# Performance work log

Hardware: AMD Instinct MI355X
Metric: run time of the kernel (lower is better)

Reference implementation:

```python
import jax, jax.numpy as jnp
import numpy as np

N_NODES = 50000
N_EDGES = 800000
D_IN, D_HID, D_OUT = 96, 96, 32


def setup_inputs() -> dict:
    key = jax.random.key(0)
    ks = jax.random.split(key, 8)
    x = jax.random.normal(ks[0], (N_NODES, D_IN), dtype=jnp.float32)
    edge_index = jax.random.randint(ks[1], (2, N_EDGES), 0, N_NODES, dtype=jnp.int64)
    # Glorot-style init for GCNConv linear weights, zero bias (PyG default)
    def glorot(k, fan_in, fan_out):
        s = jnp.sqrt(6.0 / (fan_in + fan_out))
        return jax.random.uniform(k, (fan_in, fan_out), jnp.float32, -s, s)
    return {
        "x": x,
        "edge_index": edge_index,
        "W1": glorot(ks[2], D_IN, D_HID), "b1": jnp.zeros((D_HID,), jnp.float32),
        "W2": glorot(ks[3], D_HID, D_HID), "b2": jnp.zeros((D_HID,), jnp.float32),
        "W3": glorot(ks[4], D_HID, D_OUT), "b3": jnp.zeros((D_OUT,), jnp.float32),
    }


def _gcn_conv(x, W, b, src, dst, norm, n):
    # x: [N, d_in] -> transform then normalized neighbor aggregation (incl. self-loops)
    h = x @ W                                   # [N, d_out]
    msgs = h[src] * norm[:, None]               # [E+N, d_out] gather + scale
    out = jax.ops.segment_sum(msgs, dst, num_segments=n)  # scatter-add
    return out + b


def reference(x, edge_index, W1, b1, W2, b2, W3, b3):
    n = x.shape[0]
    loop = jnp.arange(n, dtype=edge_index.dtype)
    src = jnp.concatenate([edge_index[0], loop])  # [E+N]
    dst = jnp.concatenate([edge_index[1], loop])  # [E+N]
    # symmetric GCN normalization: deg^-1/2[src] * deg^-1/2[dst] (self-loops included)
    deg = jax.ops.segment_sum(jnp.ones_like(dst, dtype=x.dtype), dst, num_segments=n)
    dinv = jnp.where(deg > 0, jax.lax.rsqrt(deg), 0.0)
    norm = dinv[src] * dinv[dst]

    h = jax.nn.relu(_gcn_conv(x, W1, b1, src, dst, norm, n))  # dropout: eval mode (identity)
    h = jax.nn.relu(_gcn_conv(h, W2, b2, src, dst, norm, n))
    return _gcn_conv(h, W3, b3, src, dst, norm, n)
```

## Files before the change

### kernel.cpp

```cpp
#include <hip/hip_runtime.h>
#include <hip/hip_bf16.h>
#include <hip/hip_fp16.h>

static constexpr int KDIM = 96;
static constexpr int BSH = 7;
static constexpr int BNODES = 1 << BSH;
static constexpr int MAXBK = 400;

typedef _Float16 f16x8 __attribute__((ext_vector_type(8)));
typedef float f32x4 __attribute__((ext_vector_type(4)));

__device__ __forceinline__ void gemm96_f32_body(const float* __restrict__ x,
                                                const float* __restrict__ Wg,
                                                __half* __restrict__ out, int N,
                                                int gb, char* sm) {
  _Float16* Wt = (_Float16*)sm;
  const int tid = threadIdx.x;
  for (int i = tid; i < 96 * 96; i += 256) {
    int k = i / 96, j = i - k * 96;
    Wt[j * 104 + k] = (_Float16)Wg[i];
  }
  __syncthreads();
  const int wave = tid >> 6;
  const int l = tid & 63;
  const int crow = l & 15;
  const int kgrp = l >> 4;
  int r = gb * 64 + wave * 16 + crow;
  int rc = (r < N) ? r : (N - 1);
  f16x8 a[3];
  const float* ap = x + (size_t)rc * 96 + kgrp * 8;
#pragma unroll
  for (int ks = 0; ks < 3; ++ks) {
    float4 u = *(const float4*)(ap + ks * 32);
    float4 w = *(const float4*)(ap + ks * 32 + 4);
    a[ks][0] = (_Float16)u.x; a[ks][1] = (_Float16)u.y;
    a[ks][2] = (_Float16)u.z; a[ks][3] = (_Float16)u.w;
    a[ks][4] = (_Float16)w.x; a[ks][5] = (_Float16)w.y;
    a[ks][6] = (_Float16)w.z; a[ks][7] = (_Float16)w.w;
  }
  const int rbase = gb * 64 + wave * 16 + kgrp * 4;
#pragma unroll
  for (int nt = 0; nt < 6; ++nt) {
    f32x4 c = {0.f, 0.f, 0.f, 0.f};
#pragma unroll
    for (int ks = 0; ks < 3; ++ks) {
      f16x8 b = *(const f16x8*)&Wt[(nt * 16 + crow) * 104 + ks * 32 + kgrp * 8];
      c = __builtin_amdgcn_mfma_f32_16x16x32_f16(a[ks], b, c, 0, 0, 0);
    }
#pragma unroll
    for (int reg = 0; reg < 4; ++reg) {
      int R = rbase + reg;
      if (R < N) out[(size_t)R * 96 + nt * 16 + crow] = (__half)c[reg];
    }
  }
}

__global__ __launch_bounds__(256) void khist_gemm1(const int* __restrict__ dst,
                                                   int* __restrict__ gbcnt,
                                                   int E, int NBK,
                                                   const float* __restrict__ x,
                                                   const float* __restrict__ W1,
                                                   __half* __restrict__ tA, int N,
                                                   const float* __restrict__ W2,
                                                   const float* __restrict__ W3,
                                                   _Float16* __restrict__ Wt2,
                                                   _Float16* __restrict__ Wt3,
                                                   int gG) {
  __shared__ __align__(16) char sm[96 * 104 * 2];
  if (blockIdx.x < 256) {
    int* h = (int*)sm;
    for (int i = threadIdx.x; i < NBK; i += 256) h[i] = 0;
    __syncthreads();
    for (int e = blockIdx.x * 256 + threadIdx.x; e < E; e += 256 * 256)
      atomicAdd(&h[dst[e] >> BSH], 1);
    __syncthreads();
    for (int i = threadIdx.x; i < NBK; i += 256)
      if (h[i]) atomicAdd(&gbcnt[i], h[i]);
  } else if (blockIdx.x < 256 + gG) {
    gemm96_f32_body(x, W1, tA, N, blockIdx.x - 256, sm);
  } else {
    for (int i = threadIdx.x; i < 96 * 96; i += 256) {
      int k = i / 96, j = i - k * 96;
      Wt2[j * 96 + k] = (_Float16)W2[i];
    }
    for (int i = threadIdx.x; i < 96 * 32; i += 256) {
      int k = i / 32, j = i - k * 32;
      Wt3[j * 96 + k] = (_Float16)W3[i];
    }
  }
}

__global__ void kb_scanb(const int* __restrict__ gbcnt, int* __restrict__ bstart,
                         int* __restrict__ bcur, int NBK) {
  __shared__ int s[512];
  int t = threadIdx.x;
  int v = (t < NBK) ? gbcnt[t] : 0;
  s[t] = v;
  __syncthreads();
  for (int o = 1; o < 512; o <<= 1) {
    int a = (t >= o) ? s[t - o] : 0;
    __syncthreads();
    s[t] += a;
    __syncthreads();
  }
  if (t < NBK) {
    int excl = s[t] - v;
    bstart[t] = excl;
    bcur[t] = excl;
  }
  if (t == 511) bstart[NBK] = s[511];
}

__global__ __launch_bounds__(256) void kb_scatter(const int* __restrict__ src,
                                                  const int* __restrict__ dst,
                                                  int* __restrict__ bcur,
                                                  unsigned* __restrict__ tmp,
                                                  int E, int NBK, int chunk) {
  __shared__ int h[MAXBK];
  __shared__ int base[MAXBK];
  int lo = blockIdx.x * chunk;
  int hi = min(lo + chunk, E);
  for (int i = threadIdx.x; i < NBK; i += 256) h[i] = 0;
  __syncthreads();
  for (int e = lo + threadIdx.x; e < hi; e += 256) atomicAdd(&h[dst[e] >> BSH], 1);
  __syncthreads();
  for (int i = threadIdx.x; i < NBK; i += 256) {
    int c = h[i];
    base[i] = c ? atomicAdd(&bcur[i], c) : 0;
    h[i] = 0;
  }
  __syncthreads();
  for (int e = lo + threadIdx.x; e < hi; e += 256) {
    int d = dst[e];
    int b = d >> BSH;
    int p = base[b] + atomicAdd(&h[b], 1);
    tmp[p] = (unsigned)src[e] | ((unsigned)(d & (BNODES - 1)) << 16);
  }
}

__global__ __launch_bounds__(256) void kb_cnt2(const unsigned* __restrict__ tmp,
                                               const int* __restrict__ bstart,
                                               int* __restrict__ cursor,
                                               float* __restrict__ dinv,
                                               int2* __restrict__ rs, int N) {
  __shared__ int hcnt[BNODES];
  __shared__ int scn[BNODES];
  __shared__ int gbs;
  int b = blockIdx.x;
  int t = threadIdx.x;
  for (int i = t; i < BNODES; i += 256) hcnt[i] = 0;
  __syncthreads();
  int lo = bstart[b], hi = bstart[b + 1];
  for (int p = lo + t; p < hi; p += 256)
    atomicAdd(&hcnt[(tmp[p] >> 16) & (BNODES - 1)], 1);
  __syncthreads();
  int pcnt = 0;
  if (t < BNODES) {
    pcnt = (hcnt[t] + 3) & ~3;
    scn[t] = pcnt;
  }
  __syncthreads();
  for (int o = 1; o < BNODES; o <<= 1) {
    int a = (t < BNODES && t >= o) ? scn[t - o] : 0;
    __syncthreads();
    if (t < BNODES) scn[t] += a;
    __syncthreads();
  }
  if (t == 0) gbs = atomicAdd(cursor, scn[BNODES - 1]);
  __syncthreads();
  if (t < BNODES) {
    int v = (b << BSH) + t;
    if (v < N) {
      int beg = gbs + scn[t] - pcnt;
      rs[v] = make_int2(beg, beg + pcnt);
      dinv[v] = rsqrtf((float)hcnt[t] + 1.0f);
    }
  }
}

__global__ __launch_bounds__(256) void kb_final2(const unsigned* __restrict__ tmp,
                                                 const int* __restrict__ bstart,
                                                 const int2* __restrict__ rs,
                                                 const float* __restrict__ dinv,
                                                 unsigned* __restrict__ ew, int N) {
  __shared__ int beg[BNODES];
  __shared__ int endp[BNODES];
  __shared__ int lcur[BNODES];
  int b = blockIdx.x;
  int t = threadIdx.x;
  int v0 = b << BSH;
  if (t < BNODES) {
    int v = v0 + t;
    if (v < N) {
      int2 r = rs[v];
      beg[t] = r.x;
      endp[t] = r.y;
    } else {
      beg[t] = 0;
      endp[t] = 0;
    }
    lcur[t] = 0;
  }
  __syncthreads();
  int lo = bstart[b], hi = bstart[b + 1];
  for (int p = lo + t; p < hi; p += 256) {
    unsigned u = tmp[p];
    int dl = (u >> 16) & (BNODES - 1);
    int s = u & 0xFFFF;
    int pos = beg[dl] + atomicAdd(&lcur[dl], 1);
    unsigned hw = (unsigned)__half_as_ushort(__float2half(dinv[s]));
    ew[pos] = (unsigned)s | (hw << 16);
  }
  __syncthreads();
  if (t < BNODES) {
    int p = beg[t] + lcur[t];
    int end = endp[t];
    for (; p < end; ++p) ew[p] = 0u;
  }
}

template <int DOUT>
__global__ __launch_bounds__(256) void kfuse(const __half* __restrict__ t,
                                             const int2* __restrict__ rs,
                                             const unsigned* __restrict__ ew,
                                             const float* __restrict__ dinv,
                                             const float* __restrict__ bias,
                                             const _Float16* __restrict__ Wt,
                                             __half* __restrict__ out, int N) {
  __shared__ _Float16 A[16 * 104];
  const int tid = threadIdx.x;
  const int wave = tid >> 6;
  const int lane = tid & 63;
  const int li = (lane < 48) ? lane : 47;
  const int fb = li << 2;
  const char* tb = (const char*)t;
  const float bx = bias[2 * li];
  const float by = bias[2 * li + 1];
#pragma unroll
  for (int i = 0; i < 4; ++i) {
    int row = wave * 4 + i;
    int v = blockIdx.x * 16 + row;
    if (v < N) {
      float dv = dinv[v];
      float2 acc;
      {
        __half2 r = *(const __half2*)(tb + (size_t)v * 192 + fb);
        float2 f = __half22float2(r);
        acc.x = dv * f.x;
        acc.y = dv * f.y;
      }
      int2 range = rs[v];
      int e = range.x;
      const int e1 = range.y;
      for (; e < e1; e += 4) {
        uint4 q = *(const uint4*)(ew + e);
        __half2 r0 = *(const __half2*)(tb + (size_t)(q.x & 0xFFFF) * 192 + fb);
        __half2 r1 = *(const __half2*)(tb + (size_t)(q.y & 0xFFFF) * 192 + fb);
        __half2 r2 = *(const __half2*)(tb + (size_t)(q.z & 0xFFFF) * 192 + fb);
        __half2 r3 = *(const __half2*)(tb + (size_t)(q.w & 0xFFFF) * 192 + fb);
        float2 a0 = __half22float2(r0), a1 = __half22float2(r1);
        float2 a2 = __half22float2(r2), a3 = __half22float2(r3);
        float w0 = __half2float(__ushort_as_half((unsigned short)(q.x >> 16)));
        float w1 = __half2float(__ushort_as_half((unsigned short)(q.y >> 16)));
        float w2 = __half2float(__ushort_as_half((unsigned short)(q.z >> 16)));
        float w3 = __half2float(__ushort_as_half((unsigned short)(q.w >> 16)));
        acc.x = fmaf(w0, a0.x, acc.x); acc.y = fmaf(w0, a0.y, acc.y);
        acc.x = fmaf(w1, a1.x, acc.x); acc.y = fmaf(w1, a1.y, acc.y);
        acc.x = fmaf(w2, a2.x, acc.x); acc.y = fmaf(w2, a2.y, acc.y);
        acc.x = fmaf(w3, a3.x, acc.x); acc.y = fmaf(w3, a3.y, acc.y);
      }
      if (lane < 48) {
        float rx = fmaxf(fmaf(dv, acc.x, bx), 0.f);
        float ry = fmaxf(fmaf(dv, acc.y, by), 0.f);
        A[row * 104 + 2 * li] = (_Float16)rx;
        A[row * 104 + 2 * li + 1] = (_Float16)ry;
      }
    }
  }
  __syncthreads();
  const int crow = lane & 15;
  const int kgrp = lane >> 4;
  f16x8 a[3];
  const _Float16* arow = &A[crow * 104 + kgrp * 8];
#pragma unroll
  for (int ks = 0; ks < 3; ++ks) a[ks] = *(const f16x8*)(arow + ks * 32);
  const int rbase = blockIdx.x * 16 + kgrp * 4;
#pragma unroll
  for (int w2 = 0; w2 < 2; ++w2) {
    int nt = wave + 4 * w2;
    if (nt >= DOUT / 16) break;
    f32x4 c = {0.f, 0.f, 0.f, 0.f};
#pragma unroll
    for (int ks = 0; ks < 3; ++ks) {
      f16x8 b = *(const f16x8*)&Wt[(nt * 16 + crow) * 96 + ks * 32 + kgrp * 8];
      c = __builtin_amdgcn_mfma_f32_16x16x32_f16(a[ks], b, c, 0, 0, 0);
    }
#pragma unroll
    for (int reg = 0; reg < 4; ++reg) {
      int R = rbase + reg;
      if (R < N) out[(size_t)R * DOUT + nt * 16 + crow] = (__half)c[reg];
    }
  }
}

__global__ __launch_bounds__(256) void k_agg32h(const __half* __restrict__ t,
                                                const int2* __restrict__ rs,
                                                const unsigned* __restrict__ ew,
                                                const float* __restrict__ dinv,
                                                const float* __restrict__ bias,
                                                float* __restrict__ out, int N) {
  int half = threadIdx.x >> 5;
  int lane = threadIdx.x & 31;
  int v = blockIdx.x * 8 + half;
  if (v >= N) return;
  const char* tb = (const char*)t;
  const int fb = lane << 1;
  float dv = dinv[v];
  float acc = dv * __half2float(*(const __half*)(tb + (size_t)v * 64 + fb));
  int2 range = rs[v];
  int e = range.x;
  const int e1 = range.y;
  for (; e < e1; e += 4) {
    uint4 q = *(const uint4*)(ew + e);
    float a0 = __half2float(*(const __half*)(tb + (size_t)(q.x & 0xFFFF) * 64 + fb));
    float a1 = __half2float(*(const __half*)(tb + (size_t)(q.y & 0xFFFF) * 64 + fb));
    float a2 = __half2float(*(const __half*)(tb + (size_t)(q.z & 0xFFFF) * 64 + fb));
    float a3 = __half2float(*(const __half*)(tb + (size_t)(q.w & 0xFFFF) * 64 + fb));
    acc = fmaf(__half2float(__ushort_as_half((unsigned short)(q.x >> 16))), a0, acc);
    acc = fmaf(__half2float(__ushort_as_half((unsigned short)(q.y >> 16))), a1, acc);
    acc = fmaf(__half2float(__ushort_as_half((unsigned short)(q.z >> 16))), a2, acc);
    acc = fmaf(__half2float(__ushort_as_half((unsigned short)(q.w >> 16))), a3, acc);
  }
  out[(size_t)v * 32 + lane] = fmaf(dv, acc, bias[lane]);
}


extern "C" void kernel_launch(void* const* d_in, const int* in_sizes, int n_in,
                              void* d_out, int out_size, void* d_ws, size_t ws_size,
                              hipStream_t stream) {
  const float* x  = (const float*)d_in[0];
  const int*   ei = (const int*)d_in[1];
  const float* W1 = (const float*)d_in[2];
  const float* b1 = (const float*)d_in[3];
  const float* W2 = (const float*)d_in[4];
  const float* b2 = (const float*)d_in[5];
  const float* W3 = (const float*)d_in[6];
  const float* b3 = (const float*)d_in[7];
  float* out = (float*)d_out;

  const int N = in_sizes[0] / KDIM;
  const int E = in_sizes[1] / 2;
  const int* src = ei;
  const int* dst = ei + E;
  const int NBK = (N + BNODES - 1) >> BSH;

  char* w = (char*)d_ws;
  size_t off = 0;
  auto alloc = [&](size_t bytes) {
    char* p = w + off;
    off = (off + bytes + 255) & ~(size_t)255;
    return p;
  };
  int*       gbcnt    = (int*)alloc((size_t)(MAXBK + 8) * 4);
  int*       bstart   = (int*)alloc((size_t)(MAXBK + 1) * 4);
  int*       bcur     = (int*)alloc((size_t)MAXBK * 4);
  float*     dinv     = (float*)alloc((size_t)N * 4);
  int2*      rs       = (int2*)alloc((size_t)N * 8);
  unsigned*  tmp      = (unsigned*)alloc((size_t)E * 4);
  unsigned*  ew       = (unsigned*)alloc((size_t)(E + 4 * (size_t)N + 16) * 4);
  __half*    tA       = (__half*)alloc((size_t)N * KDIM * 2);
  __half*    tB       = (__half*)alloc((size_t)N * KDIM * 2);
  __half*    tC       = (__half*)alloc((size_t)N * 32 * 2);
  _Float16*  Wt2      = (_Float16*)alloc((size_t)96 * 96 * 2);
  _Float16*  Wt3      = (_Float16*)alloc((size_t)32 * 96 * 2);
  int*       cursor   = gbcnt + MAXBK;

  hipMemsetAsync(gbcnt, 0, (size_t)(MAXBK + 8) * 4, stream);

  const int NCH = 512;
  const int chunk = (E + NCH - 1) / NCH;
  const int gG = (N + 63) / 64;
  const int gF = (N + 15) / 16;
  const int gA8 = (N + 7) / 8;

  khist_gemm1<<<256 + gG + 1, 256, 0, stream>>>(dst, gbcnt, E, NBK, x, W1, tA, N,
                                                W2, W3, Wt2, Wt3, gG);
  kb_scanb<<<1, 512, 0, stream>>>(gbcnt, bstart, bcur, NBK);
  kb_scatter<<<NCH, 256, 0, stream>>>(src, dst, bcur, tmp, E, NBK, chunk);
  kb_cnt2<<<NBK, 256, 0, stream>>>(tmp, bstart, cursor, dinv, rs, N);
  kb_final2<<<NBK, 256, 0, stream>>>(tmp, bstart, rs, dinv, ew, N);

  kfuse<96><<<gF, 256, 0, stream>>>(tA, rs, ew, dinv, b1, Wt2, tB, N);
  kfuse<32><<<gF, 256, 0, stream>>>(tB, rs, ew, dinv, b2, Wt3, tC, N);
  k_agg32h<<<gA8, 256, 0, stream>>>(tC, rs, ew, dinv, b3, out, N);
}
```

Baseline: 161.5 us.

## Replace bucket histogram+scan with fixed-capacity buckets and global per-node counts

Removes the separate bucket histogram, scan, and count kernels by scattering edges directly into fixed-capacity per-bucket regions (CAP slots each). Per-node degrees come from global atomics during the scatter, which is fused with the first GEMM launch. A per-256-node scan kernel then builds row starts. This cuts three launches and one pass over the edge list, at the cost of heavy global atomic traffic on node counters. It also risks overflow if a bucket ever exceeds CAP edges.

```diff
diff --git a/kernel.cpp b/kernel.cpp
--- a/kernel.cpp
+++ b/kernel.cpp
@@ -6,6 +6,7 @@
 static constexpr int BSH = 7;
 static constexpr int BNODES = 1 << BSH;
 static constexpr int MAXBK = 400;
+static constexpr int CAP = 4096;
 
 typedef _Float16 f16x8 __attribute__((ext_vector_type(8)));
 typedef float f32x4 __attribute__((ext_vector_type(4)));
@@ -55,29 +56,43 @@
   }
 }
 
-__global__ __launch_bounds__(256) void khist_gemm1(const int* __restrict__ dst,
-                                                   int* __restrict__ gbcnt,
-                                                   int E, int NBK,
-                                                   const float* __restrict__ x,
-                                                   const float* __restrict__ W1,
-                                                   __half* __restrict__ tA, int N,
-                                                   const float* __restrict__ W2,
-                                                   const float* __restrict__ W3,
-                                                   _Float16* __restrict__ Wt2,
-                                                   _Float16* __restrict__ Wt3,
-                                                   int gG) {
+__global__ __launch_bounds__(256) void ksca_gemm1(
+    const int* __restrict__ src, const int* __restrict__ dst,
+    int* __restrict__ cnt, int* __restrict__ bcur, unsigned* __restrict__ tmp,
+    int E, int NBK, int chunk,
+    const float* __restrict__ x, const float* __restrict__ W1,
+    __half* __restrict__ tA, int N,
+    const float* __restrict__ W2, const float* __restrict__ W3,
+    _Float16* __restrict__ Wt2, _Float16* __restrict__ Wt3,
+    int NCH, int gG) {
   __shared__ __align__(16) char sm[96 * 104 * 2];
-  if (blockIdx.x < 256) {
+  if (blockIdx.x < (unsigned)NCH) {
     int* h = (int*)sm;
+    int* base = h + MAXBK;
+    int lo = blockIdx.x * chunk;
+    int hi = min(lo + chunk, E);
     for (int i = threadIdx.x; i < NBK; i += 256) h[i] = 0;
     __syncthreads();
-    for (int e = blockIdx.x * 256 + threadIdx.x; e < E; e += 256 * 256)
-      atomicAdd(&h[dst[e] >> BSH], 1);
-    __syncthreads();
-    for (int i = threadIdx.x; i < NBK; i += 256)
-      if (h[i]) atomicAdd(&gbcnt[i], h[i]);
-  } else if (blockIdx.x < 256 + gG) {
-    gemm96_f32_body(x, W1, tA, N, blockIdx.x - 256, sm);
+    for (int e = lo + threadIdx.x; e < hi; e += 256) {
+      int d = dst[e];
+      atomicAdd(&h[d >> BSH], 1);
+      atomicAdd(&cnt[d], 1);
+    }
+    __syncthreads();
+    for (int i = threadIdx.x; i < NBK; i += 256) {
+      int c = h[i];
+      base[i] = c ? (i * CAP + atomicAdd(&bcur[i], c)) : 0;
+      h[i] = 0;
+    }
+    __syncthreads();
+    for (int e = lo + threadIdx.x; e < hi; e += 256) {
+      int d = dst[e];
+      int b = d >> BSH;
+      int p = base[b] + atomicAdd(&h[b], 1);
+      tmp[p] = (unsigned)src[e] | ((unsigned)(d & (BNODES - 1)) << 16);
+    }
+  } else if (blockIdx.x < (unsigned)(NCH + gG)) {
+    gemm96_f32_body(x, W1, tA, N, blockIdx.x - NCH, sm);
   } else {
     for (int i = threadIdx.x; i < 96 * 96; i += 256) {
       int k = i / 96, j = i - k * 96;
@@ -90,96 +105,35 @@
   }
 }
 
-__global__ void kb_scanb(const int* __restrict__ gbcnt, int* __restrict__ bstart,
-                         int* __restrict__ bcur, int NBK) {
-  __shared__ int s[512];
+__global__ __launch_bounds__(256) void k_rs(const int* __restrict__ cnt,
+                                            int* __restrict__ cursor,
+                                            float* __restrict__ dinv,
+                                            int2* __restrict__ rs, int N) {
+  __shared__ int scn[256];
+  __shared__ int gbs;
   int t = threadIdx.x;
-  int v = (t < NBK) ? gbcnt[t] : 0;
-  s[t] = v;
-  __syncthreads();
-  for (int o = 1; o < 512; o <<= 1) {
-    int a = (t >= o) ? s[t - o] : 0;
-    __syncthreads();
-    s[t] += a;
-    __syncthreads();
-  }
-  if (t < NBK) {
-    int excl = s[t] - v;
-    bstart[t] = excl;
-    bcur[t] = excl;
-  }
-  if (t == 511) bstart[NBK] = s[511];
-}
-
-__global__ __launch_bounds__(256) void kb_scatter(const int* __restrict__ src,
-                                                  const int* __restrict__ dst,
-                                                  int* __restrict__ bcur,
-                                                  unsigned* __restrict__ tmp,
-                                                  int E, int NBK, int chunk) {
-  __shared__ int h[MAXBK];
-  __shared__ int base[MAXBK];
-  int lo = blockIdx.x * chunk;
-  int hi = min(lo + chunk, E);
-  for (int i = threadIdx.x; i < NBK; i += 256) h[i] = 0;
-  __syncthreads();
-  for (int e = lo + threadIdx.x; e < hi; e += 256) atomicAdd(&h[dst[e] >> BSH], 1);
-  __syncthreads();
-  for (int i = threadIdx.x; i < NBK; i += 256) {
-    int c = h[i];
-    base[i] = c ? atomicAdd(&bcur[i], c) : 0;
-    h[i] = 0;
-  }
-  __syncthreads();
-  for (int e = lo + threadIdx.x; e < hi; e += 256) {
-    int d = dst[e];
-    int b = d >> BSH;
-    int p = base[b] + atomicAdd(&h[b], 1);
-    tmp[p] = (unsigned)src[e] | ((unsigned)(d & (BNODES - 1)) << 16);
-  }
-}
-
-__global__ __launch_bounds__(256) void kb_cnt2(const unsigned* __restrict__ tmp,
-                                               const int* __restrict__ bstart,
-                                               int* __restrict__ cursor,
-                                               float* __restrict__ dinv,
-                                               int2* __restrict__ rs, int N) {
-  __shared__ int hcnt[BNODES];
-  __shared__ int scn[BNODES];
-  __shared__ int gbs;
-  int b = blockIdx.x;
-  int t = threadIdx.x;
-  for (int i = t; i < BNODES; i += 256) hcnt[i] = 0;
-  __syncthreads();
-  int lo = bstart[b], hi = bstart[b + 1];
-  for (int p = lo + t; p < hi; p += 256)
-    atomicAdd(&hcnt[(tmp[p] >> 16) & (BNODES - 1)], 1);
-  __syncthreads();
-  int pcnt = 0;
-  if (t < BNODES) {
-    pcnt = (hcnt[t] + 3) & ~3;
-    scn[t] = pcnt;
-  }
-  __syncthreads();
-  for (int o = 1; o < BNODES; o <<= 1) {
-    int a = (t < BNODES && t >= o) ? scn[t - o] : 0;
-    __syncthreads();
-    if (t < BNODES) scn[t] += a;
-    __syncthreads();
-  }
-  if (t == 0) gbs = atomicAdd(cursor, scn[BNODES - 1]);
-  __syncthreads();
-  if (t < BNODES) {
-    int v = (b << BSH) + t;
-    if (v < N) {
-      int beg = gbs + scn[t] - pcnt;
-      rs[v] = make_int2(beg, beg + pcnt);
-      dinv[v] = rsqrtf((float)hcnt[t] + 1.0f);
-    }
-  }
-}
-
-__global__ __launch_bounds__(256) void kb_final2(const unsigned* __restrict__ tmp,
-                                                 const int* __restrict__ bstart,
+  int v = blockIdx.x * 256 + t;
+  int c = (v < N) ? cnt[v] : 0;
+  int p = (c + 3) & ~3;
+  scn[t] = p;
+  __syncthreads();
+  for (int o = 1; o < 256; o <<= 1) {
+    int a = (t >= o) ? scn[t - o] : 0;
+    __syncthreads();
+    scn[t] += a;
+    __syncthreads();
+  }
+  if (t == 0) gbs = atomicAdd(cursor, scn[255]);
+  __syncthreads();
+  if (v < N) {
+    int beg = gbs + scn[t] - p;
+    rs[v] = make_int2(beg, beg + p);
+    dinv[v] = rsqrtf((float)c + 1.0f);
+  }
+}
+
+__global__ __launch_bounds__(256) void kb_final3(const unsigned* __restrict__ tmp,
+                                                 const int* __restrict__ bcur,
                                                  const int2* __restrict__ rs,
                                                  const float* __restrict__ dinv,
                                                  unsigned* __restrict__ ew, int N) {
@@ -202,9 +156,10 @@
     lcur[t] = 0;
   }
   __syncthreads();
-  int lo = bstart[b], hi = bstart[b + 1];
-  for (int p = lo + t; p < hi; p += 256) {
-    unsigned u = tmp[p];
+  const unsigned* tb = tmp + (size_t)b * CAP;
+  int cntb = bcur[b];
+  for (int p = t; p < cntb; p += 256) {
+    unsigned u = tb[p];
     int dl = (u >> 16) & (BNODES - 1);
     int s = u & 0xFFFF;
     int pos = beg[dl] + atomicAdd(&lcur[dl], 1);
@@ -361,21 +316,21 @@
     off = (off + bytes + 255) & ~(size_t)255;
     return p;
   };
-  int*       gbcnt    = (int*)alloc((size_t)(MAXBK + 8) * 4);
-  int*       bstart   = (int*)alloc((size_t)(MAXBK + 1) * 4);
-  int*       bcur     = (int*)alloc((size_t)MAXBK * 4);
+  int*       meta     = (int*)alloc((size_t)(MAXBK + 8 + N) * 4);
+  int*       bcur     = meta;
+  int*       cursor   = meta + MAXBK;
+  int*       cnt      = meta + MAXBK + 8;
   float*     dinv     = (float*)alloc((size_t)N * 4);
   int2*      rs       = (int2*)alloc((size_t)N * 8);
-  unsigned*  tmp      = (unsigned*)alloc((size_t)E * 4);
+  unsigned*  tmp      = (unsigned*)alloc((size_t)MAXBK * CAP * 4);
   unsigned*  ew       = (unsigned*)alloc((size_t)(E + 4 * (size_t)N + 16) * 4);
   __half*    tA       = (__half*)alloc((size_t)N * KDIM * 2);
   __half*    tB       = (__half*)alloc((size_t)N * KDIM * 2);
   __half*    tC       = (__half*)alloc((size_t)N * 32 * 2);
   _Float16*  Wt2      = (_Float16*)alloc((size_t)96 * 96 * 2);
   _Float16*  Wt3      = (_Float16*)alloc((size_t)32 * 96 * 2);
-  int*       cursor   = gbcnt + MAXBK;
-
-  hipMemsetAsync(gbcnt, 0, (size_t)(MAXBK + 8) * 4, stream);
+
+  hipMemsetAsync(meta, 0, (size_t)(MAXBK + 8 + N) * 4, stream);
 
   const int NCH = 512;
   const int chunk = (E + NCH - 1) / NCH;
@@ -383,12 +338,11 @@
   const int gF = (N + 15) / 16;
   const int gA8 = (N + 7) / 8;
 
-  khist_gemm1<<<256 + gG + 1, 256, 0, stream>>>(dst, gbcnt, E, NBK, x, W1, tA, N,
-                                                W2, W3, Wt2, Wt3, gG);
-  kb_scanb<<<1, 512, 0, stream>>>(gbcnt, bstart, bcur, NBK);
-  kb_scatter<<<NCH, 256, 0, stream>>>(src, dst, bcur, tmp, E, NBK, chunk);
-  kb_cnt2<<<NBK, 256, 0, stream>>>(tmp, bstart, cursor, dinv, rs, N);
-  kb_final2<<<NBK, 256, 0, stream>>>(tmp, bstart, rs, dinv, ew, N);
+  ksca_gemm1<<<NCH + gG + 1, 256, 0, stream>>>(src, dst, cnt, bcur, tmp, E, NBK,
+                                               chunk, x, W1, tA, N, W2, W3, Wt2,
+                                               Wt3, NCH, gG);
+  k_rs<<<(N + 255) / 256, 256, 0, stream>>>(cnt, cursor, dinv, rs, N);
+  kb_final3<<<NBK, 256, 0, stream>>>(tmp, bcur, rs, dinv, ew, N);
 
   kfuse<96><<<gF, 256, 0, stream>>>(tA, rs, ew, dinv, b1, Wt2, tB, N);
   kfuse<32><<<gF, 256, 0, stream>>>(tB, rs, ew, dinv, b2, Wt3, tC, N);
```

Measured after the change: 179.0 us. +10.9%, slower.

## Fuse CSR build kernels and shrink edge list to 16-bit indices

Applied to the files above, without the earlier changes.

Merges the count and fill kernels into one build kernel, which drops a launch and a second pass over the bucketed temp array. The packed 32-bit edge entries (source index plus half-precision source weight) become bare 16-bit source indices. Aggregation kernels now look up the source normalisation in a small half-precision dinv table. Padding slots point at sentinel node N, whose weight is zero, and the feature buffers get an extra row for it. This halves edge-list traffic at the cost of an extra cached gather per edge; the sentinel feature rows are never initialised, so a NaN there could leak through the zero weight.

```diff
diff --git a/kernel.cpp b/kernel.cpp
--- a/kernel.cpp
+++ b/kernel.cpp
@@ -91,7 +91,8 @@
 }
 
 __global__ void kb_scanb(const int* __restrict__ gbcnt, int* __restrict__ bstart,
-                         int* __restrict__ bcur, int NBK) {
+                         int* __restrict__ bcur, int NBK,
+                         __half* __restrict__ dinv16, int N) {
   __shared__ int s[512];
   int t = threadIdx.x;
   int v = (t < NBK) ? gbcnt[t] : 0;
@@ -109,6 +110,7 @@
     bcur[t] = excl;
   }
   if (t == 511) bstart[NBK] = s[511];
+  if (t == 0) dinv16[N] = __ushort_as_half((unsigned short)0);
 }
 
 __global__ __launch_bounds__(256) void kb_scatter(const int* __restrict__ src,
@@ -138,13 +140,18 @@
   }
 }
 
-__global__ __launch_bounds__(256) void kb_cnt2(const unsigned* __restrict__ tmp,
-                                               const int* __restrict__ bstart,
-                                               int* __restrict__ cursor,
-                                               float* __restrict__ dinv,
-                                               int2* __restrict__ rs, int N) {
+__global__ __launch_bounds__(256) void kb_build(const unsigned* __restrict__ tmp,
+                                                const int* __restrict__ bstart,
+                                                int* __restrict__ cursor,
+                                                float* __restrict__ dinv,
+                                                __half* __restrict__ dinv16,
+                                                int2* __restrict__ rs,
+                                                unsigned short* __restrict__ ew,
+                                                int N) {
   __shared__ int hcnt[BNODES];
   __shared__ int scn[BNODES];
+  __shared__ int beg[BNODES];
+  __shared__ int lcur[BNODES];
   __shared__ int gbs;
   int b = blockIdx.x;
   int t = threadIdx.x;
@@ -170,60 +177,37 @@
   __syncthreads();
   if (t < BNODES) {
     int v = (b << BSH) + t;
+    int bg = gbs + scn[t] - pcnt;
+    beg[t] = bg;
+    lcur[t] = 0;
     if (v < N) {
-      int beg = gbs + scn[t] - pcnt;
-      rs[v] = make_int2(beg, beg + pcnt);
-      dinv[v] = rsqrtf((float)hcnt[t] + 1.0f);
-    }
-  }
-}
-
-__global__ __launch_bounds__(256) void kb_final2(const unsigned* __restrict__ tmp,
-                                                 const int* __restrict__ bstart,
-                                                 const int2* __restrict__ rs,
-                                                 const float* __restrict__ dinv,
-                                                 unsigned* __restrict__ ew, int N) {
-  __shared__ int beg[BNODES];
-  __shared__ int endp[BNODES];
-  __shared__ int lcur[BNODES];
-  int b = blockIdx.x;
-  int t = threadIdx.x;
-  int v0 = b << BSH;
-  if (t < BNODES) {
-    int v = v0 + t;
-    if (v < N) {
-      int2 r = rs[v];
-      beg[t] = r.x;
-      endp[t] = r.y;
-    } else {
-      beg[t] = 0;
-      endp[t] = 0;
-    }
-    lcur[t] = 0;
-  }
-  __syncthreads();
-  int lo = bstart[b], hi = bstart[b + 1];
+      rs[v] = make_int2(bg, bg + pcnt);
+      float di = rsqrtf((float)hcnt[t] + 1.0f);
+      dinv[v] = di;
+      dinv16[v] = __float2half(di);
+    }
+  }
+  __syncthreads();
   for (int p = lo + t; p < hi; p += 256) {
     unsigned u = tmp[p];
     int dl = (u >> 16) & (BNODES - 1);
-    int s = u & 0xFFFF;
     int pos = beg[dl] + atomicAdd(&lcur[dl], 1);
-    unsigned hw = (unsigned)__half_as_ushort(__float2half(dinv[s]));
-    ew[pos] = (unsigned)s | (hw << 16);
+    ew[pos] = (unsigned short)(u & 0xFFFF);
   }
   __syncthreads();
   if (t < BNODES) {
     int p = beg[t] + lcur[t];
-    int end = endp[t];
-    for (; p < end; ++p) ew[p] = 0u;
+    int end = beg[t] + ((hcnt[t] + 3) & ~3);
+    for (; p < end; ++p) ew[p] = (unsigned short)N;
   }
 }
 
 template <int DOUT>
 __global__ __launch_bounds__(256) void kfuse(const __half* __restrict__ t,
                                              const int2* __restrict__ rs,
-                                             const unsigned* __restrict__ ew,
+                                             const unsigned short* __restrict__ ew,
                                              const float* __restrict__ dinv,
+                                             const __half* __restrict__ dinv16,
                                              const float* __restrict__ bias,
                                              const _Float16* __restrict__ Wt,
                                              __half* __restrict__ out, int N) {
@@ -253,17 +237,17 @@
       int e = range.x;
       const int e1 = range.y;
       for (; e < e1; e += 4) {
-        uint4 q = *(const uint4*)(ew + e);
-        __half2 r0 = *(const __half2*)(tb + (size_t)(q.x & 0xFFFF) * 192 + fb);
-        __half2 r1 = *(const __half2*)(tb + (size_t)(q.y & 0xFFFF) * 192 + fb);
-        __half2 r2 = *(const __half2*)(tb + (size_t)(q.z & 0xFFFF) * 192 + fb);
-        __half2 r3 = *(const __half2*)(tb + (size_t)(q.w & 0xFFFF) * 192 + fb);
+        ushort4 q = *(const ushort4*)(ew + e);
+        __half2 r0 = *(const __half2*)(tb + (size_t)q.x * 192 + fb);
+        __half2 r1 = *(const __half2*)(tb + (size_t)q.y * 192 + fb);
+        __half2 r2 = *(const __half2*)(tb + (size_t)q.z * 192 + fb);
+        __half2 r3 = *(const __half2*)(tb + (size_t)q.w * 192 + fb);
+        float w0 = __half2float(dinv16[q.x]);
+        float w1 = __half2float(dinv16[q.y]);
+        float w2 = __half2float(dinv16[q.z]);
+        float w3 = __half2float(dinv16[q.w]);
         float2 a0 = __half22float2(r0), a1 = __half22float2(r1);
         float2 a2 = __half22float2(r2), a3 = __half22float2(r3);
-        float w0 = __half2float(__ushort_as_half((unsigned short)(q.x >> 16)));
-        float w1 = __half2float(__ushort_as_half((unsigned short)(q.y >> 16)));
-        float w2 = __half2float(__ushort_as_half((unsigned short)(q.z >> 16)));
-        float w3 = __half2float(__ushort_as_half((unsigned short)(q.w >> 16)));
         acc.x = fmaf(w0, a0.x, acc.x); acc.y = fmaf(w0, a0.y, acc.y);
         acc.x = fmaf(w1, a1.x, acc.x); acc.y = fmaf(w1, a1.y, acc.y);
         acc.x = fmaf(w2, a2.x, acc.x); acc.y = fmaf(w2, a2.y, acc.y);
@@ -305,8 +289,9 @@
 
 __global__ __launch_bounds__(256) void k_agg32h(const __half* __restrict__ t,
                                                 const int2* __restrict__ rs,
-                                                const unsigned* __restrict__ ew,
+                                                const unsigned short* __restrict__ ew,
                                                 const float* __restrict__ dinv,
+                                                const __half* __restrict__ dinv16,
                                                 const float* __restrict__ bias,
                                                 float* __restrict__ out, int N) {
   int half = threadIdx.x >> 5;
@@ -321,15 +306,15 @@
   int e = range.x;
   const int e1 = range.y;
   for (; e < e1; e += 4) {
-    uint4 q = *(const uint4*)(ew + e);
-    float a0 = __half2float(*(const __half*)(tb + (size_t)(q.x & 0xFFFF) * 64 + fb));
-    float a1 = __half2float(*(const __half*)(tb + (size_t)(q.y & 0xFFFF) * 64 + fb));
-    float a2 = __half2float(*(const __half*)(tb + (size_t)(q.z & 0xFFFF) * 64 + fb));
-    float a3 = __half2float(*(const __half*)(tb + (size_t)(q.w & 0xFFFF) * 64 + fb));
-    acc = fmaf(__half2float(__ushort_as_half((unsigned short)(q.x >> 16))), a0, acc);
-    acc = fmaf(__half2float(__ushort_as_half((unsigned short)(q.y >> 16))), a1, acc);
-    acc = fmaf(__half2float(__ushort_as_half((unsigned short)(q.z >> 16))), a2, acc);
-    acc = fmaf(__half2float(__ushort_as_half((unsigned short)(q.w >> 16))), a3, acc);
+    ushort4 q = *(const ushort4*)(ew + e);
+    float a0 = __half2float(*(const __half*)(tb + (size_t)q.x * 64 + fb));
+    float a1 = __half2float(*(const __half*)(tb + (size_t)q.y * 64 + fb));
+    float a2 = __half2float(*(const __half*)(tb + (size_t)q.z * 64 + fb));
+    float a3 = __half2float(*(const __half*)(tb + (size_t)q.w * 64 + fb));
+    acc = fmaf(__half2float(dinv16[q.x]), a0, acc);
+    acc = fmaf(__half2float(dinv16[q.y]), a1, acc);
+    acc = fmaf(__half2float(dinv16[q.z]), a2, acc);
+    acc = fmaf(__half2float(dinv16[q.w]), a3, acc);
   }
   out[(size_t)v * 32 + lane] = fmaf(dv, acc, bias[lane]);
 }
@@ -361,19 +346,20 @@
     off = (off + bytes + 255) & ~(size_t)255;
     return p;
   };
-  int*       gbcnt    = (int*)alloc((size_t)(MAXBK + 8) * 4);
-  int*       bstart   = (int*)alloc((size_t)(MAXBK + 1) * 4);
-  int*       bcur     = (int*)alloc((size_t)MAXBK * 4);
-  float*     dinv     = (float*)alloc((size_t)N * 4);
-  int2*      rs       = (int2*)alloc((size_t)N * 8);
-  unsigned*  tmp      = (unsigned*)alloc((size_t)E * 4);
-  unsigned*  ew       = (unsigned*)alloc((size_t)(E + 4 * (size_t)N + 16) * 4);
-  __half*    tA       = (__half*)alloc((size_t)N * KDIM * 2);
-  __half*    tB       = (__half*)alloc((size_t)N * KDIM * 2);
-  __half*    tC       = (__half*)alloc((size_t)N * 32 * 2);
-  _Float16*  Wt2      = (_Float16*)alloc((size_t)96 * 96 * 2);
-  _Float16*  Wt3      = (_Float16*)alloc((size_t)32 * 96 * 2);
-  int*       cursor   = gbcnt + MAXBK;
+  int*            gbcnt  = (int*)alloc((size_t)(MAXBK + 8) * 4);
+  int*            bstart = (int*)alloc((size_t)(MAXBK + 1) * 4);
+  int*            bcur   = (int*)alloc((size_t)MAXBK * 4);
+  float*          dinv   = (float*)alloc((size_t)N * 4);
+  __half*         dinv16 = (__half*)alloc((size_t)(N + 1) * 2);
+  int2*           rs     = (int2*)alloc((size_t)N * 8);
+  unsigned*       tmp    = (unsigned*)alloc((size_t)E * 4);
+  unsigned short* ew     = (unsigned short*)alloc((size_t)(E + 4 * (size_t)N + 16) * 2);
+  __half*         tA     = (__half*)alloc((size_t)(N + 1) * KDIM * 2);
+  __half*         tB     = (__half*)alloc((size_t)(N + 1) * KDIM * 2);
+  __half*         tC     = (__half*)alloc((size_t)(N + 1) * 32 * 2);
+  _Float16*       Wt2    = (_Float16*)alloc((size_t)96 * 96 * 2);
+  _Float16*       Wt3    = (_Float16*)alloc((size_t)32 * 96 * 2);
+  int*            cursor = gbcnt + MAXBK;
 
   hipMemsetAsync(gbcnt, 0, (size_t)(MAXBK + 8) * 4, stream);
 
@@ -385,12 +371,11 @@
 
   khist_gemm1<<<256 + gG + 1, 256, 0, stream>>>(dst, gbcnt, E, NBK, x, W1, tA, N,
                                                 W2, W3, Wt2, Wt3, gG);
-  kb_scanb<<<1, 512, 0, stream>>>(gbcnt, bstart, bcur, NBK);
+  kb_scanb<<<1, 512, 0, stream>>>(gbcnt, bstart, bcur, NBK, dinv16, N);
   kb_scatter<<<NCH, 256, 0, stream>>>(src, dst, bcur, tmp, E, NBK, chunk);
-  kb_cnt2<<<NBK, 256, 0, stream>>>(tmp, bstart, cursor, dinv, rs, N);
-  kb_final2<<<NBK, 256, 0, stream>>>(tmp, bstart, rs, dinv, ew, N);
-
-  kfuse<96><<<gF, 256, 0, stream>>>(tA, rs, ew, dinv, b1, Wt2, tB, N);
-  kfuse<32><<<gF, 256, 0, stream>>>(tB, rs, ew, dinv, b2, Wt3, tC, N);
-  k_agg32h<<<gA8, 256, 0, stream>>>(tC, rs, ew, dinv, b3, out, N);
-}
+  kb_build<<<NBK, 256, 0, stream>>>(tmp, bstart, cursor, dinv, dinv16, rs, ew, N);
+
+  kfuse<96><<<gF, 256, 0, stream>>>(tA, rs, ew, dinv, dinv16, b1, Wt2, tB, N);
+  kfuse<32><<<gF, 256, 0, stream>>>(tB, rs, ew, dinv, dinv16, b2, Wt3, tC, N);
+  k_agg32h<<<gA8, 256, 0, stream>>>(tC, rs, ew, dinv, dinv16, b3, out, N);
+}
```

New measurement: 162.0 us. No clear change (+0.3%).
